# Kernel optimization log

Hardware: AMD Instinct MI355X
Metric: run time of the kernel (lower is better)

Reference implementation:

```python
import jax, jax.numpy as jnp
import numpy as np

S, L = 4096, 12
VOCAB, CHARS, TAGS = 100000, 128, 64
CE, CH, WE, H = 64, 128, 256, 512


def setup_inputs() -> dict:
    key = jax.random.key(0)
    ks = jax.random.split(key, 16)
    n = lambda k, shp, s=0.05: (jax.random.normal(k, shp, jnp.float32) * s)
    return {
        "w_seq": jax.random.randint(ks[0], (S,), 0, VOCAB),
        "c_seq": jax.random.randint(ks[1], (S, L), 0, CHARS),
        "char_emb": n(ks[2], (CHARS, CE), 1.0),
        "word_emb": n(ks[3], (VOCAB, WE), 1.0),
        "c_hx0": jnp.zeros((CH,), jnp.float32),
        "c_cx0": jnp.zeros((CH,), jnp.float32),
        "hx0": jnp.zeros((H,), jnp.float32),
        "cx0": jnp.zeros((H,), jnp.float32),
        "Wih1": n(ks[4], (4 * CH, CE)),
        "Whh1": n(ks[5], (4 * CH, CH)),
        "bih1": n(ks[6], (4 * CH,)),
        "bhh1": n(ks[7], (4 * CH,)),
        "Wih2": n(ks[8], (4 * H, WE + CH)),
        "Whh2": n(ks[9], (4 * H, H)),
        "bih2": n(ks[10], (4 * H,)),
        "bhh2": n(ks[11], (4 * H,)),
        "W_out": n(ks[12], (TAGS, H)),
        "b_out": n(ks[13], (TAGS,)),
    }


def _lstm_step(x, h, c, Wih, Whh, b):
    # PyTorch gate order: i, f, g, o
    g = x @ Wih.T + h @ Whh.T + b
    i, f, gg, o = jnp.split(g, 4, axis=-1)
    c = jax.nn.sigmoid(f) * c + jax.nn.sigmoid(i) * jnp.tanh(gg)
    h = jax.nn.sigmoid(o) * jnp.tanh(c)
    return h, c


def reference(w_seq, c_seq, char_emb, word_emb, c_hx0, c_cx0, hx0, cx0,
              Wih1, Whh1, bih1, bhh1, Wih2, Whh2, bih2, bhh2, W_out, b_out):
    nwords = w_seq.shape[0]
    # --- batched per-word char LSTM (all words run as one batch) ---
    xs = jnp.transpose(char_emb[c_seq], (1, 0, 2))  # [L, S, CE]
    b1 = bih1 + bhh1
    h0 = jnp.broadcast_to(c_hx0, (nwords, c_hx0.shape[0]))
    c0 = jnp.broadcast_to(c_cx0, (nwords, c_cx0.shape[0]))

    def step1(carry, x):
        h, c = _lstm_step(x, carry[0], carry[1], Wih1, Whh1, b1)
        return (h, c), None

    (char_rep, _), _ = jax.lax.scan(step1, (h0, c0), xs)  # [S, CH]

    # --- word-level LSTM over the sentence ---
    wv = word_emb[w_seq]                                  # [S, WE]
    seq = jnp.concatenate([char_rep, wv], axis=1)         # [S, CH+WE]
    b2 = bih2 + bhh2

    def step2(carry, x):
        h, c = _lstm_step(x, carry[0], carry[1], Wih2, Whh2, b2)
        return (h, c), h

    _, outs = jax.lax.scan(step2, (hx0, cx0), seq)        # [S, H]

    tag_space = outs @ W_out.T + b_out                    # [S, TAGS]
    return jax.nn.log_softmax(tag_space, axis=1)
```

## Files before the change

### kernel.cpp

```cpp
#include <hip/hip_runtime.h>
#include <math.h>

#define S_LEN 4096
#define L_CH  12
#define CE    64
#define CHD   128
#define WE    256
#define HD    512
#define TAGS  64
#define GW    (4*HD)
#define XDIM  (CHD+WE)
#define NBLK  64

#define WS_GX    0
#define WS_CREP  (WS_GX   + (size_t)S_LEN*GW)
#define WS_HEXT  (WS_CREP + (size_t)S_LEN*CHD)

typedef float v4f __attribute__((ext_vector_type(4)));

static __device__ __forceinline__ float sigf(float x) {
    return 1.0f / (1.0f + __expf(-x));
}
static __device__ __forceinline__ float tanhfast(float x) {
    return 1.0f - 2.0f / (__expf(2.0f * x) + 1.0f);
}

__global__ __launch_bounds__(256) void k_init(const float* __restrict__ hx0,
                                              float* __restrict__ hext) {
    size_t i = ((size_t)blockIdx.x * 256 + threadIdx.x) * 4;
    if (i >= (size_t)(S_LEN + 1) * HD) return;
    v4f v;
    if (i < HD) {
        v.x = hx0[i+0] + 2.0f; v.y = hx0[i+1] + 2.0f;
        v.z = hx0[i+2] + 2.0f; v.w = hx0[i+3] + 2.0f;
    } else {
        v.x = 0.f; v.y = 0.f; v.z = 0.f; v.w = 0.f;
    }
    float* p = hext + i;
    asm volatile("global_store_dwordx4 %0, %1, off sc0 sc1"
                 :: "v"(p), "v"(v) : "memory");
}

__global__ __launch_bounds__(256) void k_char_lstm(
    const int* __restrict__ c_seq, const float* __restrict__ char_emb,
    const float* __restrict__ c_hx0, const float* __restrict__ c_cx0,
    const float* __restrict__ Wih1, const float* __restrict__ Whh1,
    const float* __restrict__ bih1, const float* __restrict__ bhh1,
    float* __restrict__ char_rep)
{
    __shared__ float xs[16][CE + 4];
    __shared__ float hs[16][CHD + 4];
    __shared__ float cs[16][CHD + 4];
    __shared__ float gs[16][4*CHD + 4];
    const int tid = threadIdx.x;
    const int w0  = blockIdx.x * 16;

    for (int u = tid; u < 16*CHD; u += 256) {
        int w = u >> 7, k = u & (CHD-1);
        hs[w][k] = c_hx0[k];
        cs[w][k] = c_cx0[k];
    }
    __syncthreads();

    const int wg = tid & 3;
    const int rg = tid >> 2;
    const int uw = tid >> 4;
    const int uj = (tid & 15) * 8;

    for (int t = 0; t < L_CH; ++t) {
        {
            int w = tid >> 4, k4 = (tid & 15) * 4;
            int ci = c_seq[(w0 + w) * L_CH + t];
            float4 v = *(const float4*)(char_emb + (size_t)ci * CE + k4);
            *(float4*)&xs[w][k4] = v;
        }
        __syncthreads();

        float acc[8][4];
        #pragma unroll
        for (int i = 0; i < 8; ++i)
            #pragma unroll
            for (int j = 0; j < 4; ++j) acc[i][j] = 0.0f;

        for (int kc = 0; kc < CE/4; ++kc) {
            int k = kc * 4;
            float4 xv[4];
            #pragma unroll
            for (int j = 0; j < 4; ++j) xv[j] = *(const float4*)&xs[wg*4 + j][k];
            #pragma unroll
            for (int i = 0; i < 8; ++i) {
                int r = rg*8 + i;
                float4 wv = *(const float4*)(Wih1 + (size_t)r*CE + k);
                #pragma unroll
                for (int j = 0; j < 4; ++j)
                    acc[i][j] += wv.x*xv[j].x + wv.y*xv[j].y + wv.z*xv[j].z + wv.w*xv[j].w;
            }
        }
        for (int kc = 0; kc < CHD/4; ++kc) {
            int k = kc * 4;
            float4 hv[4];
            #pragma unroll
            for (int j = 0; j < 4; ++j) hv[j] = *(const float4*)&hs[wg*4 + j][k];
            #pragma unroll
            for (int i = 0; i < 8; ++i) {
                int r = rg*8 + i;
                float4 wv = *(const float4*)(Whh1 + (size_t)r*CHD + k);
                #pragma unroll
                for (int j = 0; j < 4; ++j)
                    acc[i][j] += wv.x*hv[j].x + wv.y*hv[j].y + wv.z*hv[j].z + wv.w*hv[j].w;
            }
        }
        #pragma unroll
        for (int i = 0; i < 8; ++i) {
            int r = rg*8 + i;
            float b = bih1[r] + bhh1[r];
            #pragma unroll
            for (int j = 0; j < 4; ++j) gs[wg*4 + j][r] = acc[i][j] + b;
        }
        __syncthreads();

        #pragma unroll
        for (int i = 0; i < 8; ++i) {
            int j = uj + i;
            float gi = gs[uw][j];
            float gf = gs[uw][CHD + j];
            float gg = gs[uw][2*CHD + j];
            float go = gs[uw][3*CHD + j];
            float c = sigf(gf)*cs[uw][j] + sigf(gi)*tanhfast(gg);
            cs[uw][j] = c;
            hs[uw][j] = sigf(go)*tanhfast(c);
        }
        __syncthreads();
    }
    #pragma unroll
    for (int i4 = 0; i4 < 2; ++i4) {
        float4 v;
        v.x = hs[uw][uj + i4*4 + 0]; v.y = hs[uw][uj + i4*4 + 1];
        v.z = hs[uw][uj + i4*4 + 2]; v.w = hs[uw][uj + i4*4 + 3];
        *(float4*)(char_rep + (size_t)(w0 + uw)*CHD + uj + i4*4) = v;
    }
}

__global__ __launch_bounds__(256) void k_gx(
    const int* __restrict__ w_seq, const float* __restrict__ word_emb,
    const float* __restrict__ char_rep,
    const float* __restrict__ Wih2, const float* __restrict__ bih2,
    const float* __restrict__ bhh2, float* __restrict__ Gx)
{
    __shared__ float xs[16][XDIM + 4];
    const int tid = threadIdx.x;
    const int w0  = blockIdx.x * 16;
    const int slice = blockIdx.y;

    {
        int w = tid >> 4, seg = tid & 15;
        int wsq = w_seq[w0 + w];
        #pragma unroll
        for (int i4 = 0; i4 < 6; ++i4) {
            int k = seg*24 + i4*4;
            float4 v;
            if (k < CHD) v = *(const float4*)(char_rep + (size_t)(w0+w)*CHD + k);
            else         v = *(const float4*)(word_emb + (size_t)wsq*WE + (k - CHD));
            *(float4*)&xs[w][k] = v;
        }
    }
    __syncthreads();

    const int wg = tid & 3, rg = tid >> 2;
    float acc[8][4];
    #pragma unroll
    for (int i = 0; i < 8; ++i)
        #pragma unroll
        for (int j = 0; j < 4; ++j) acc[i][j] = 0.0f;

    for (int kc = 0; kc < XDIM/4; ++kc) {
        int k = kc * 4;
        float4 xv[4];
        #pragma unroll
        for (int j = 0; j < 4; ++j) xv[j] = *(const float4*)&xs[wg*4 + j][k];
        #pragma unroll
        for (int i = 0; i < 8; ++i) {
            int r = slice*512 + rg*8 + i;
            float4 wv = *(const float4*)(Wih2 + (size_t)r*XDIM + k);
            #pragma unroll
            for (int j = 0; j < 4; ++j)
                acc[i][j] += wv.x*xv[j].x + wv.y*xv[j].y + wv.z*xv[j].z + wv.w*xv[j].w;
        }
    }
    #pragma unroll
    for (int i = 0; i < 8; ++i) {
        int r = slice*512 + rg*8 + i;
        float b = bih2[r] + bhh2[r];
        #pragma unroll
        for (int j = 0; j < 4; ++j)
            Gx[(size_t)(w0 + wg*4 + j)*GW + r] = acc[i][j] + b;
    }
}

__global__ __launch_bounds__(256, 1) void k_word_lstm(
    const float* __restrict__ Gx, const float* __restrict__ Whh2,
    const float* __restrict__ cx0, float* __restrict__ hext)
{
    const int tid  = threadIdx.x;
    const int b    = blockIdx.x;
    const int hb   = b * 8;
    const int w    = tid >> 6;
    const int lane = tid & 63;
    const int jj   = lane & 1;
    const int s    = lane >> 1;
    const int ks   = s * 16;
    const int jo   = hb + w*2 + jj;

    float wreg[4][16];
    float wsum[4];
    #pragma unroll
    for (int q = 0; q < 4; ++q) {
        const float* wr = Whh2 + (size_t)(q*HD + jo)*HD + ks;
        float ssum = 0.0f;
        #pragma unroll
        for (int m4 = 0; m4 < 4; ++m4) {
            float4 v = *(const float4*)(wr + m4*4);
            wreg[q][m4*4+0] = v.x; wreg[q][m4*4+1] = v.y;
            wreg[q][m4*4+2] = v.z; wreg[q][m4*4+3] = v.w;
            ssum += v.x + v.y + v.z + v.w;
        }
        wsum[q] = 2.0f * ssum;
    }
    float creg = (s == 0) ? cx0[jo] : 0.0f;

    for (int t = 0; t < S_LEN; ++t) {
        float gx0 = 0.f, gx1 = 0.f, gx2 = 0.f, gx3 = 0.f;
        if (s == 0) {
            const float* gp = Gx + (size_t)t*GW + jo;
            gx0 = gp[0]; gx1 = gp[HD]; gx2 = gp[2*HD]; gx3 = gp[3*HD];
        }

        const float* hsrc = hext + (size_t)t*HD + ks;
        v4f r0, r1, r2, r3;
        for (;;) {
            asm volatile(
                "global_load_dwordx4 %0, %4, off sc0 sc1\n\t"
                "global_load_dwordx4 %1, %4, off offset:16 sc0 sc1\n\t"
                "global_load_dwordx4 %2, %4, off offset:32 sc0 sc1\n\t"
                "global_load_dwordx4 %3, %4, off offset:48 sc0 sc1\n\t"
                "s_waitcnt vmcnt(0)"
                : "=&v"(r0), "=&v"(r1), "=&v"(r2), "=&v"(r3)
                : "v"(hsrc)
                : "memory");
            float mn = fminf(fminf(fminf(r0.x, r0.y), fminf(r0.z, r0.w)),
                             fminf(fminf(r1.x, r1.y), fminf(r1.z, r1.w)));
            mn = fminf(mn, fminf(fminf(fminf(r2.x, r2.y), fminf(r2.z, r2.w)),
                                 fminf(fminf(r3.x, r3.y), fminf(r3.z, r3.w))));
            if (__all(mn > 0.5f)) break;
            __builtin_amdgcn_s_sleep(1);
        }

        float hv[16];
        hv[0]=r0.x; hv[1]=r0.y; hv[2]=r0.z; hv[3]=r0.w;
        hv[4]=r1.x; hv[5]=r1.y; hv[6]=r1.z; hv[7]=r1.w;
        hv[8]=r2.x; hv[9]=r2.y; hv[10]=r2.z; hv[11]=r2.w;
        hv[12]=r3.x; hv[13]=r3.y; hv[14]=r3.z; hv[15]=r3.w;

        float a0 = 0.f, a1 = 0.f, a2 = 0.f, a3 = 0.f;
        #pragma unroll
        for (int m = 0; m < 16; ++m) {
            a0 += wreg[0][m] * hv[m];
            a1 += wreg[1][m] * hv[m];
            a2 += wreg[2][m] * hv[m];
            a3 += wreg[3][m] * hv[m];
        }
        a0 -= wsum[0]; a1 -= wsum[1]; a2 -= wsum[2]; a3 -= wsum[3];

        #pragma unroll
        for (int off = 2; off < 64; off <<= 1) {
            a0 += __shfl_xor(a0, off, 64);
            a1 += __shfl_xor(a1, off, 64);
            a2 += __shfl_xor(a2, off, 64);
            a3 += __shfl_xor(a3, off, 64);
        }

        if (s == 0) {
            float g0 = gx0 + a0, g1 = gx1 + a1, g2 = gx2 + a2, g3 = gx3 + a3;
            float c  = sigf(g1)*creg + sigf(g0)*tanhfast(g2);
            creg = c;
            float hn = sigf(g3)*tanhfast(c) + 2.0f;
            float* dst = hext + (size_t)(t+1)*HD + jo;
            asm volatile("global_store_dword %0, %1, off sc0 sc1"
                         :: "v"(dst), "v"(hn) : "memory");
        }
    }
}

__global__ __launch_bounds__(256) void k_out(
    const float* __restrict__ outs_b, const float* __restrict__ W_out,
    const float* __restrict__ b_out, float* __restrict__ out)
{
    __shared__ float hh[16][HD + 4];
    __shared__ float ts[16][TAGS + 4];
    __shared__ float lse[16];
    const int tid = threadIdx.x;
    const int w0  = blockIdx.x * 16;

    {
        int w = tid >> 4, k0 = (tid & 15) * 32;
        #pragma unroll
        for (int i4 = 0; i4 < 8; ++i4) {
            float4 v = *(const float4*)(outs_b + (size_t)(w0+w)*HD + k0 + i4*4);
            int k = k0 + i4*4;
            hh[w][k+0] = v.x - 2.0f; hh[w][k+1] = v.y - 2.0f;
            hh[w][k+2] = v.z - 2.0f; hh[w][k+3] = v.w - 2.0f;
        }
    }
    __syncthreads();

    const int tag = tid & 63;
    const int wg  = tid >> 6;
    float a0 = 0.f, a1 = 0.f, a2 = 0.f, a3 = 0.f;
    for (int kc = 0; kc < HD/4; ++kc) {
        int k = kc * 4;
        float4 wv = *(const float4*)(W_out + (size_t)tag*HD + k);
        float4 x0 = *(const float4*)&hh[wg*4+0][k];
        float4 x1 = *(const float4*)&hh[wg*4+1][k];
        float4 x2 = *(const float4*)&hh[wg*4+2][k];
        float4 x3 = *(const float4*)&hh[wg*4+3][k];
        a0 += wv.x*x0.x + wv.y*x0.y + wv.z*x0.z + wv.w*x0.w;
        a1 += wv.x*x1.x + wv.y*x1.y + wv.z*x1.z + wv.w*x1.w;
        a2 += wv.x*x2.x + wv.y*x2.y + wv.z*x2.z + wv.w*x2.w;
        a3 += wv.x*x3.x + wv.y*x3.y + wv.z*x3.z + wv.w*x3.w;
    }
    float bo = b_out[tag];
    ts[wg*4+0][tag] = a0 + bo;
    ts[wg*4+1][tag] = a1 + bo;
    ts[wg*4+2][tag] = a2 + bo;
    ts[wg*4+3][tag] = a3 + bo;
    __syncthreads();

    if (tid < 16) {
        float m = -1e30f;
        for (int q = 0; q < TAGS; ++q) m = fmaxf(m, ts[tid][q]);
        float ssum = 0.0f;
        for (int q = 0; q < TAGS; ++q) ssum += __expf(ts[tid][q] - m);
        lse[tid] = m + __logf(ssum);
    }
    __syncthreads();

    #pragma unroll
    for (int jjj = 0; jjj < 4; ++jjj)
        out[(size_t)(w0 + wg*4 + jjj)*TAGS + tag] = ts[wg*4+jjj][tag] - lse[wg*4+jjj];
}

extern "C" void kernel_launch(void* const* d_in, const int* in_sizes, int n_in,
                              void* d_out, int out_size, void* d_ws, size_t ws_size,
                              hipStream_t stream) {
    (void)in_sizes; (void)n_in; (void)out_size; (void)ws_size;
    const int*   w_seq    = (const int*)  d_in[0];
    const int*   c_seq    = (const int*)  d_in[1];
    const float* char_emb = (const float*)d_in[2];
    const float* word_emb = (const float*)d_in[3];
    const float* c_hx0    = (const float*)d_in[4];
    const float* c_cx0    = (const float*)d_in[5];
    const float* hx0      = (const float*)d_in[6];
    const float* cx0      = (const float*)d_in[7];
    const float* Wih1     = (const float*)d_in[8];
    const float* Whh1     = (const float*)d_in[9];
    const float* bih1     = (const float*)d_in[10];
    const float* bhh1     = (const float*)d_in[11];
    const float* Wih2     = (const float*)d_in[12];
    const float* Whh2     = (const float*)d_in[13];
    const float* bih2     = (const float*)d_in[14];
    const float* bhh2     = (const float*)d_in[15];
    const float* W_out    = (const float*)d_in[16];
    const float* b_out    = (const float*)d_in[17];

    float* ws   = (float*)d_ws;
    float* Gx   = ws + WS_GX;
    float* crep = ws + WS_CREP;
    float* hext = ws + WS_HEXT;

    int init_blocks = (int)(((size_t)(S_LEN + 1) * HD / 4 + 255) / 256);
    hipLaunchKernelGGL(k_init, dim3(init_blocks), dim3(256), 0, stream, hx0, hext);
    hipLaunchKernelGGL(k_char_lstm, dim3(256), dim3(256), 0, stream,
                       c_seq, char_emb, c_hx0, c_cx0, Wih1, Whh1, bih1, bhh1, crep);
    hipLaunchKernelGGL(k_gx, dim3(256, 4), dim3(256), 0, stream,
                       w_seq, word_emb, crep, Wih2, bih2, bhh2, Gx);
    hipLaunchKernelGGL(k_word_lstm, dim3(NBLK), dim3(256), 0, stream,
                       Gx, Whh2, cx0, hext);
    hipLaunchKernelGGL(k_out, dim3(256), dim3(256), 0, stream,
                       hext + HD, W_out, b_out, (float*)d_out);
}
```

Before: 10.63 ms.

## Remap word LSTM to one hidden unit per wave with DPP reductions

The recurrent word-LSTM kernel now gives each wave a single hidden unit across 128 blocks instead of 64. Each half-wave covers two gates over the full 512-wide hidden state. The cross-lane reduction uses DPP row shifts, row broadcast and readlane instead of shfl_xor butterflies, and the s_sleep in the spin-wait poll is dropped. The aim is a shorter per-timestep critical path (fewer FMAs per lane, cheaper reductions, faster wake on new h), at the cost of more polling blocks competing on the shared h flags.

```diff
diff --git a/kernel.cpp b/kernel.cpp
--- a/kernel.cpp
+++ b/kernel.cpp
@@ -10,7 +10,7 @@
 #define TAGS  64
 #define GW    (4*HD)
 #define XDIM  (CHD+WE)
-#define NBLK  64
+#define NBLK  128
 
 #define WS_GX    0
 #define WS_CREP  (WS_GX   + (size_t)S_LEN*GW)
@@ -23,6 +23,17 @@
 }
 static __device__ __forceinline__ float tanhfast(float x) {
     return 1.0f - 2.0f / (__expf(2.0f * x) + 1.0f);
+}
+static __device__ __forceinline__ float dot4(v4f a, v4f b) {
+    return a.x*b.x + a.y*b.y + a.z*b.z + a.w*b.w;
+}
+template <int CTRL, int RMASK>
+static __device__ __forceinline__ float dpp_add(float a) {
+    int t = __builtin_amdgcn_update_dpp(0, __float_as_int(a), CTRL, RMASK, 0xf, true);
+    return a + __int_as_float(t);
+}
+static __device__ __forceinline__ float rdlane(float v, int l) {
+    return __int_as_float(__builtin_amdgcn_readlane(__float_as_int(v), l));
 }
 
 __global__ __launch_bounds__(256) void k_init(const float* __restrict__ hx0,
@@ -202,40 +213,42 @@
     const float* __restrict__ cx0, float* __restrict__ hext)
 {
     const int tid  = threadIdx.x;
-    const int b    = blockIdx.x;
-    const int hb   = b * 8;
     const int w    = tid >> 6;
     const int lane = tid & 63;
-    const int jj   = lane & 1;
-    const int s    = lane >> 1;
-    const int ks   = s * 16;
-    const int jo   = hb + w*2 + jj;
-
-    float wreg[4][16];
-    float wsum[4];
-    #pragma unroll
-    for (int q = 0; q < 4; ++q) {
-        const float* wr = Whh2 + (size_t)(q*HD + jo)*HD + ks;
-        float ssum = 0.0f;
-        #pragma unroll
-        for (int m4 = 0; m4 < 4; ++m4) {
-            float4 v = *(const float4*)(wr + m4*4);
-            wreg[q][m4*4+0] = v.x; wreg[q][m4*4+1] = v.y;
-            wreg[q][m4*4+2] = v.z; wreg[q][m4*4+3] = v.w;
-            ssum += v.x + v.y + v.z + v.w;
-        }
-        wsum[q] = 2.0f * ssum;
-    }
-    float creg = (s == 0) ? cx0[jo] : 0.0f;
+    const int jo   = blockIdx.x * 4 + w;
+    const int g2   = lane >> 5;
+    const int qe   = g2 * 2, qo = qe + 1;
+    const int kk   = (lane & 31) * 16;
+
+    v4f we0, we1, we2, we3, wo0, wo1, wo2, wo3;
+    {
+        const float* wre = Whh2 + (size_t)(qe*HD + jo)*HD + kk;
+        const float* wro = Whh2 + (size_t)(qo*HD + jo)*HD + kk;
+        asm volatile(
+            "global_load_dwordx4 %0, %8, off\n\t"
+            "global_load_dwordx4 %1, %8, off offset:16\n\t"
+            "global_load_dwordx4 %2, %8, off offset:32\n\t"
+            "global_load_dwordx4 %3, %8, off offset:48\n\t"
+            "global_load_dwordx4 %4, %9, off\n\t"
+            "global_load_dwordx4 %5, %9, off offset:16\n\t"
+            "global_load_dwordx4 %6, %9, off offset:32\n\t"
+            "global_load_dwordx4 %7, %9, off offset:48\n\t"
+            "s_waitcnt vmcnt(0)"
+            : "=&v"(we0), "=&v"(we1), "=&v"(we2), "=&v"(we3),
+              "=&v"(wo0), "=&v"(wo1), "=&v"(wo2), "=&v"(wo3)
+            : "v"(wre), "v"(wro));
+    }
+    const float wsum_e = 2.0f * (we0.x+we0.y+we0.z+we0.w + we1.x+we1.y+we1.z+we1.w
+                               + we2.x+we2.y+we2.z+we2.w + we3.x+we3.y+we3.z+we3.w);
+    const float wsum_o = 2.0f * (wo0.x+wo0.y+wo0.z+wo0.w + wo1.x+wo1.y+wo1.z+wo1.w
+                               + wo2.x+wo2.y+wo2.z+wo2.w + wo3.x+wo3.y+wo3.z+wo3.w);
+    float creg = cx0[jo];
 
     for (int t = 0; t < S_LEN; ++t) {
-        float gx0 = 0.f, gx1 = 0.f, gx2 = 0.f, gx3 = 0.f;
-        if (s == 0) {
-            const float* gp = Gx + (size_t)t*GW + jo;
-            gx0 = gp[0]; gx1 = gp[HD]; gx2 = gp[2*HD]; gx3 = gp[3*HD];
-        }
-
-        const float* hsrc = hext + (size_t)t*HD + ks;
+        const float* gp = Gx + (size_t)t*GW + jo;
+        float gx0 = gp[0], gx1 = gp[HD], gx2 = gp[2*HD], gx3 = gp[3*HD];
+
+        const float* hsrc = hext + (size_t)t*HD + kk;
         v4f r0, r1, r2, r3;
         for (;;) {
             asm volatile(
@@ -252,38 +265,25 @@
             mn = fminf(mn, fminf(fminf(fminf(r2.x, r2.y), fminf(r2.z, r2.w)),
                                  fminf(fminf(r3.x, r3.y), fminf(r3.z, r3.w))));
             if (__all(mn > 0.5f)) break;
-            __builtin_amdgcn_s_sleep(1);
-        }
-
-        float hv[16];
-        hv[0]=r0.x; hv[1]=r0.y; hv[2]=r0.z; hv[3]=r0.w;
-        hv[4]=r1.x; hv[5]=r1.y; hv[6]=r1.z; hv[7]=r1.w;
-        hv[8]=r2.x; hv[9]=r2.y; hv[10]=r2.z; hv[11]=r2.w;
-        hv[12]=r3.x; hv[13]=r3.y; hv[14]=r3.z; hv[15]=r3.w;
-
-        float a0 = 0.f, a1 = 0.f, a2 = 0.f, a3 = 0.f;
-        #pragma unroll
-        for (int m = 0; m < 16; ++m) {
-            a0 += wreg[0][m] * hv[m];
-            a1 += wreg[1][m] * hv[m];
-            a2 += wreg[2][m] * hv[m];
-            a3 += wreg[3][m] * hv[m];
-        }
-        a0 -= wsum[0]; a1 -= wsum[1]; a2 -= wsum[2]; a3 -= wsum[3];
-
-        #pragma unroll
-        for (int off = 2; off < 64; off <<= 1) {
-            a0 += __shfl_xor(a0, off, 64);
-            a1 += __shfl_xor(a1, off, 64);
-            a2 += __shfl_xor(a2, off, 64);
-            a3 += __shfl_xor(a3, off, 64);
-        }
-
-        if (s == 0) {
-            float g0 = gx0 + a0, g1 = gx1 + a1, g2 = gx2 + a2, g3 = gx3 + a3;
-            float c  = sigf(g1)*creg + sigf(g0)*tanhfast(g2);
-            creg = c;
-            float hn = sigf(g3)*tanhfast(c) + 2.0f;
+        }
+
+        float ae = dot4(we0, r0) + dot4(we1, r1) + dot4(we2, r2) + dot4(we3, r3) - wsum_e;
+        float ao = dot4(wo0, r0) + dot4(wo1, r1) + dot4(wo2, r2) + dot4(wo3, r3) - wsum_o;
+
+        ae = dpp_add<0x111, 0xf>(ae); ao = dpp_add<0x111, 0xf>(ao);
+        ae = dpp_add<0x112, 0xf>(ae); ao = dpp_add<0x112, 0xf>(ao);
+        ae = dpp_add<0x114, 0xf>(ae); ao = dpp_add<0x114, 0xf>(ao);
+        ae = dpp_add<0x118, 0xf>(ae); ao = dpp_add<0x118, 0xf>(ao);
+        ae = dpp_add<0x142, 0xa>(ae); ao = dpp_add<0x142, 0xa>(ao);
+
+        float si = rdlane(ae, 31), sf = rdlane(ao, 31);
+        float sg = rdlane(ae, 63), so = rdlane(ao, 63);
+
+        float g0 = gx0 + si, g1 = gx1 + sf, g2v = gx2 + sg, g3 = gx3 + so;
+        float c  = sigf(g1)*creg + sigf(g0)*tanhfast(g2v);
+        creg = c;
+        float hn = sigf(g3)*tanhfast(c) + 2.0f;
+        if (lane == 0) {
             float* dst = hext + (size_t)(t+1)*HD + jo;
             asm volatile("global_store_dword %0, %1, off sc0 sc1"
                          :: "v"(dst), "v"(hn) : "memory");
```

New measurement: 10.56 ms. Within noise of the previous version (-0.7%).
